# Optimization experiments

Measured on AMD Instinct MI355X. Metric: run time of the kernel, lower is better.

Reference implementation:

```python
import jax, jax.numpy as jnp
import numpy as np

EPS = 1e-5

def _branch(x, W, gamma, beta):
    # 1x1 conv (no bias) + InstanceNorm2d(affine) + ReLU
    y = jnp.einsum('oc,bchw->bohw', W, x)
    mu = y.mean(axis=(2, 3), keepdims=True)
    var = y.var(axis=(2, 3), keepdims=True)
    y = (y - mu) * jax.lax.rsqrt(var + EPS)
    y = y * gamma[None, :, None, None] + beta[None, :, None, None]
    return jax.nn.relu(y)

def setup_inputs() -> dict:
    key = jax.random.key(0)
    ks = jax.random.split(key, 12)
    b, in_ch, h, w = 2, 256, 64, 64
    c = in_ch // 8
    d = dict(
        x1=jax.random.normal(ks[0], (b, in_ch, h, w), jnp.float32),
        x2=jax.random.normal(ks[1], (b, in_ch, h, w), jnp.float32),
        x3=jax.random.normal(ks[2], (b, in_ch, h, w), jnp.float32),
        W1=jax.random.normal(ks[3], (c, in_ch), jnp.float32) * (1.0 / np.sqrt(in_ch)),
        g1=jnp.ones((c,), jnp.float32), b1=jnp.zeros((c,), jnp.float32),
        W2=jax.random.normal(ks[4], (c, in_ch), jnp.float32) * (1.0 / np.sqrt(in_ch)),
        g2=jnp.ones((c,), jnp.float32), b2=jnp.zeros((c,), jnp.float32),
        W3=jax.random.normal(ks[5], (c, in_ch), jnp.float32) * (1.0 / np.sqrt(in_ch)),
        g3=jnp.ones((c,), jnp.float32), b3=jnp.zeros((c,), jnp.float32),
    )
    return d

def _forward(x1, x2, x3, W1, g1, b1, W2, g2, b2, W3, g3, b3):
    q1 = _branch(x1, W1, g1, b1); q2 = _branch(x2, W1, g1, b1); q3 = _branch(x3, W1, g1, b1)
    k1 = _branch(x1, W2, g2, b2); k2 = _branch(x2, W2, g2, b2); k3 = _branch(x3, W2, g2, b2)
    v1 = _branch(x1, W3, g3, b3); v2 = _branch(x2, W3, g3, b3); v3 = _branch(x3, W3, g3, b3)
    b_, c, h, w = q1.shape
    hw = h * w
    Q1 = q1.reshape(b_, c, hw).transpose(0, 2, 1)  # [b,hw,c]
    Q2 = q2.reshape(b_, c, hw).transpose(0, 2, 1)
    Q3 = q3.reshape(b_, c, hw).transpose(0, 2, 1)
    K1 = k1.reshape(b_, c, hw)                      # [b,c,hw]
    K2 = k2.reshape(b_, c, hw)
    K3 = k3.reshape(b_, c, hw)
    sm = lambda Q, K: jax.nn.softmax(jnp.einsum('bic,bcj->bij', Q, K), axis=-1)
    A12 = sm(Q1, K2); A21 = sm(Q2, K1); A23 = sm(Q2, K3)
    A32 = sm(Q3, K2); A13 = sm(Q1, K3)
    # ones[b,c,hw] @ A == broadcast of column-sums of A: track a [b,hw] vector
    colsum = lambda A: A.sum(axis=1)                        # [b,hw]
    step = lambda v, A: jnp.einsum('bk,bkj->bj', v, A)      # [b,hw]
    def bc(v):  # broadcast [b,hw] -> [b,c,h,w]
        return jnp.broadcast_to(v[:, None, :], (b_, c, hw)).reshape(b_, c, h, w)
    p1a = bc(step(step(step(colsum(A12), A23), A32), A21))
    p1b = bc(step(colsum(A12), A21))
    p2 = bc(step(colsum(A23), A32))
    p3a = bc(step(colsum(A12), A23))
    p3b = bc(colsum(A13))
    return (p1a, p1b, p2, p3a, p3b, v1, v2, v3)

def reference(x1, x2, x3, W1, g1, b1, W2, g2, b2, W3, g3, b3):
    return _forward(x1, x2, x3, W1, g1, b1, W2, g2, b2, W3, g3, b3)
```

## Files before the change

### kernel.cpp

```cpp
#include <hip/hip_runtime.h>

typedef unsigned short u16;
typedef u16  u16x8  __attribute__((ext_vector_type(8)));
typedef _Float16 f16x4 __attribute__((ext_vector_type(4)));
typedef _Float16 f16x8 __attribute__((ext_vector_type(8)));
typedef float f32x4 __attribute__((ext_vector_type(4)));

#define HW 4096
#define CIN 256
#define HW32 (HW * 32)
#define L2E 1.4426950408889634f

__device__ __forceinline__ float fexp2(float x) { return __builtin_amdgcn_exp2f(x); }

__global__ __launch_bounds__(256) void convert_kernel(const float* x1, const float* x2, const float* x3,
        const float* W1, const float* W2, const float* W3,
        _Float16* xh, _Float16* wh, float* mean) {
    int bx = blockIdx.x; int t = threadIdx.x;
    if (bx < 1536) {
        int xi = bx >> 9, b = (bx >> 8) & 1, c = bx & 255;
        const float* src = (xi == 0 ? x1 : xi == 1 ? x2 : x3) + (size_t)(b * CIN + c) * HW;
        _Float16* dst = xh + ((size_t)((xi * 2 + b) * CIN) + c) * HW;
        float s = 0.f;
        for (int i = t; i < 1024; i += 256) {
            f32x4 v = ((const f32x4*)src)[i];
            s += v[0] + v[1] + v[2] + v[3];
            f16x4 h;
#pragma unroll
            for (int r = 0; r < 4; ++r) h[r] = (_Float16)v[r];
            ((f16x4*)dst)[i] = h;
        }
        __shared__ float red[256];
        red[t] = s; __syncthreads();
        for (int k = 128; k; k >>= 1) { if (t < k) red[t] += red[t + k]; __syncthreads(); }
        if (t == 0) mean[(xi * 2 + b) * CIN + c] = red[0] * (1.f / HW);
    } else {
        int j = bx - 1536;
        int widx = j >> 1, half = j & 1;
        const float* wsrc = (widx == 0 ? W1 : widx == 1 ? W2 : W3) + half * 4096;
        _Float16* wdst = wh + widx * 8192 + half * 4096;
        for (int i = t; i < 1024; i += 256) {
            f32x4 v = ((const f32x4*)wsrc)[i];
            f16x4 h;
#pragma unroll
            for (int r = 0; r < 4; ++r) h[r] = (_Float16)v[r];
            ((f16x4*)wdst)[i] = h;
        }
    }
}

__global__ __launch_bounds__(256) void m2_kernel(const _Float16* xh, float* M2) {
    int xi = blockIdx.y, b = blockIdx.z;
    const _Float16* xb = xh + (size_t)(xi * 2 + b) * CIN * HW;
    int t = threadIdx.x; int wv = t >> 6; int L = t & 63; int m = L & 15; int quad = L >> 4;
    int tile = blockIdx.x * 4 + wv;
    int c1t = (tile >> 4) * 16, c2t = (tile & 15) * 16;
    const f16x8* ap = (const f16x8*)(xb + (size_t)(c1t + m) * HW + quad * 8);
    const f16x8* bp = (const f16x8*)(xb + (size_t)(c2t + m) * HW + quad * 8);
    f32x4 a0 = {0,0,0,0}, a1 = {0,0,0,0};
#pragma unroll 4
    for (int p = 0; p < 128; p += 2) {
        a0 = __builtin_amdgcn_mfma_f32_16x16x32_f16(ap[p * 4], bp[p * 4], a0, 0, 0, 0);
        a1 = __builtin_amdgcn_mfma_f32_16x16x32_f16(ap[(p + 1) * 4], bp[(p + 1) * 4], a1, 0, 0, 0);
    }
    f32x4 acc = a0 + a1;
    float* dst = M2 + ((size_t)(xi * 2 + b) * CIN) * CIN;
#pragma unroll
    for (int r = 0; r < 4; ++r)
        dst[(size_t)(c1t + quad * 4 + r) * CIN + c2t + m] = acc[r] * (1.f / HW);
}

__global__ __launch_bounds__(256) void stats_kernel(const float* M2, const float* mean,
        const float* W1, const float* W2, const float* W3,
        const float* g1, const float* g2, const float* g3,
        const float* b1, const float* b2, const float* b3, float2* afine) {
    int o = blockIdx.x; int xi = blockIdx.y; int b = blockIdx.z;
    int widx = o >> 5; int oc = o & 31;
    const float* Wp = (widx == 0 ? W1 : widx == 1 ? W2 : W3) + oc * CIN;
    const float* gp = (widx == 0 ? g1 : widx == 1 ? g2 : g3);
    const float* bp = (widx == 0 ? b1 : widx == 1 ? b2 : b3);
    int t = threadIdx.x;
    __shared__ float sW[256];
    __shared__ float red[256];
    sW[t] = Wp[t];
    __syncthreads();
    const float* m2row = M2 + ((size_t)(xi * 2 + b) * CIN + t) * CIN;
    float tv = 0.f;
    const f32x4* r4 = (const f32x4*)m2row;
#pragma unroll 4
    for (int k = 0; k < 64; ++k) {
        f32x4 mv = r4[k];
        const f32x4 wv = *(const f32x4*)&sW[k * 4];
        tv += mv[0] * wv[0] + mv[1] * wv[1] + mv[2] * wv[2] + mv[3] * wv[3];
    }
    red[t] = tv * sW[t]; __syncthreads();
    for (int k = 128; k; k >>= 1) { if (t < k) red[t] += red[t + k]; __syncthreads(); }
    float E2 = red[0]; __syncthreads();
    red[t] = sW[t] * mean[(xi * 2 + b) * CIN + t]; __syncthreads();
    for (int k = 128; k; k >>= 1) { if (t < k) red[t] += red[t + k]; __syncthreads(); }
    if (t == 0) {
        float mu = red[0];
        float var = E2 - mu * mu;
        float rsig = rsqrtf(var + 1e-5f);
        float scale = gp[oc] * rsig;
        float bias = bp[oc] - mu * scale;
        if (widx == 0) { scale *= L2E; bias *= L2E; }
        afine[(xi * 2 + b) * 96 + o] = make_float2(scale, bias);
    }
}

__global__ __launch_bounds__(256) void conv_kernel(const _Float16* xh, const _Float16* wh,
        const float2* afine, _Float16* qT, _Float16* kT, float* out) {
    int xi = blockIdx.y, b = blockIdx.z;
    const u16* xb = (const u16*)(xh + (size_t)(xi * 2 + b) * CIN * HW);
    int p0 = blockIdx.x * 64;
    __shared__ u16 lds[32 * 65 * 8];
    int t = threadIdx.x;
    {
        int pc = t & 7, cg = t >> 3;
        u16x8 a[8];
#pragma unroll
        for (int r = 0; r < 8; ++r)
            a[r] = *(const u16x8*)(xb + (size_t)(cg * 8 + r) * HW + p0 + pc * 8);
#pragma unroll
        for (int i = 0; i < 8; ++i) {
            u16x8 d;
#pragma unroll
            for (int r = 0; r < 8; ++r) d[r] = a[r][i];
            int p = pc * 8 + i; int fp = p ^ (p >> 3);
            *(u16x8*)&lds[(cg * 65 + fp) * 8] = d;
        }
    }
    __syncthreads();
    int wv = t >> 6, L = t & 63, m = L & 15, quad = L >> 4;
    int pw0 = wv * 16;
    f16x8 af[8];
    {
        int p = pw0 + m; int fp = p ^ (p >> 3);
#pragma unroll
        for (int k = 0; k < 8; ++k)
            af[k] = *(const f16x8*)&lds[((k * 4 + quad) * 65 + fp) * 8];
    }
    int xb2 = xi * 2 + b;
    for (int ot = 0; ot < 6; ++ot) {
        int o0 = ot * 16; int widx = ot >> 1;
        int o_col = o0 + m;
        f32x4 acc = {0, 0, 0, 0};
#pragma unroll
        for (int k = 0; k < 8; ++k) {
            f16x8 bfr = *(const f16x8*)(wh + (size_t)o_col * CIN + k * 32 + quad * 8);
            acc = __builtin_amdgcn_mfma_f32_16x16x32_f16(af[k], bfr, acc, 0, 0, 0);
        }
        float2 afv = afine[xb2 * 96 + o_col];
        f32x4 vals;
#pragma unroll
        for (int r = 0; r < 4; ++r) {
            float v = acc[r] * afv.x + afv.y;
            vals[r] = v > 0.f ? v : 0.f;
        }
        int prow = p0 + pw0 + quad * 4;
        if (widx < 2) {
            _Float16* dst = (widx == 0 ? qT : kT) + (size_t)xb2 * HW32;
            int cc = (o0 & 31) + m;
#pragma unroll
            for (int r = 0; r < 4; ++r)
                dst[(size_t)(prow + r) * 32 + cc] = (_Float16)vals[r];
        } else {
            float* dst = out + (size_t)(5 + xi) * 262144 + (size_t)b * 131072 + (size_t)(o_col - 64) * HW + prow;
            *(f32x4*)dst = vals;
        }
    }
}

__global__ __launch_bounds__(256) void zsweep_kernel(const _Float16* qT, const _Float16* kT,
        float2* Pz) {
    const int qxA[5] = {0, 1, 1, 2, 0};
    const int kxA[5] = {1, 0, 2, 1, 2};
    int mat = blockIdx.y, b = blockIdx.z;
    const _Float16* qb = qT + (size_t)(qxA[mat] * 2 + b) * HW32;
    const _Float16* kb = kT + (size_t)(kxA[mat] * 2 + b) * HW32;
    int bx = blockIdx.x;
    int jc = bx & 15, qblk = bx >> 4;
    int t = threadIdx.x; int wv = t >> 6; int L = t & 63; int m = L & 15; int quad = L >> 4;
    int i0 = qblk * 256 + wv * 64;
    f16x8 a[4];
#pragma unroll
    for (int tt = 0; tt < 4; ++tt)
        a[tt] = *(const f16x8*)(qb + (size_t)(i0 + tt * 16 + m) * 32 + quad * 8);
    const f16x8* kp = (const f16x8*)(kb + m * 32 + quad * 8) + (size_t)jc * (16 * 64);
    f32x4 zero = {0.f, 0.f, 0.f, 0.f};
    f32x4 mx[4] = {zero, zero, zero, zero};
#pragma unroll 4
    for (int j = 0; j < 16; ++j) {
        f16x8 bf = kp[j * 64];
#pragma unroll
        for (int tt = 0; tt < 4; ++tt) {
            f32x4 d = __builtin_amdgcn_mfma_f32_16x16x32_f16(a[tt], bf, zero, 0, 0, 0);
            mx[tt][0] = fmaxf(mx[tt][0], d[0]); mx[tt][1] = fmaxf(mx[tt][1], d[1]);
            mx[tt][2] = fmaxf(mx[tt][2], d[2]); mx[tt][3] = fmaxf(mx[tt][3], d[3]);
        }
    }
#pragma unroll
    for (int tt = 0; tt < 4; ++tt)
#pragma unroll
        for (int msk = 1; msk <= 8; msk <<= 1) {
            mx[tt][0] = fmaxf(mx[tt][0], __shfl_xor(mx[tt][0], msk));
            mx[tt][1] = fmaxf(mx[tt][1], __shfl_xor(mx[tt][1], msk));
            mx[tt][2] = fmaxf(mx[tt][2], __shfl_xor(mx[tt][2], msk));
            mx[tt][3] = fmaxf(mx[tt][3], __shfl_xor(mx[tt][3], msk));
        }
    f32x4 neg[4];
#pragma unroll
    for (int tt = 0; tt < 4; ++tt) neg[tt] = -mx[tt];
    f32x4 z[4] = {zero, zero, zero, zero};
#pragma unroll 4
    for (int j = 0; j < 16; ++j) {
        f16x8 bf = kp[j * 64];
#pragma unroll
        for (int tt = 0; tt < 4; ++tt) {
            f32x4 d = __builtin_amdgcn_mfma_f32_16x16x32_f16(a[tt], bf, neg[tt], 0, 0, 0);
            z[tt][0] += fexp2(d[0]); z[tt][1] += fexp2(d[1]);
            z[tt][2] += fexp2(d[2]); z[tt][3] += fexp2(d[3]);
        }
    }
#pragma unroll
    for (int tt = 0; tt < 4; ++tt)
#pragma unroll
        for (int msk = 1; msk <= 8; msk <<= 1) {
            z[tt][0] += __shfl_xor(z[tt][0], msk); z[tt][1] += __shfl_xor(z[tt][1], msk);
            z[tt][2] += __shfl_xor(z[tt][2], msk); z[tt][3] += __shfl_xor(z[tt][3], msk);
        }
    if (m == 0) {
        int mb = mat * 2 + b;
#pragma unroll
        for (int tt = 0; tt < 4; ++tt) {
            int row = i0 + tt * 16 + quad * 4;
#pragma unroll
            for (int r = 0; r < 4; ++r)
                Pz[((size_t)mb * 16 + jc) * HW + row + r] = make_float2(mx[tt][r], z[tt][r]);
        }
    }
}

__global__ __launch_bounds__(256) void zcombine_kernel(const float2* Pz, float* R, float* Mv, float2* Wa) {
    int mb = blockIdx.y;
    int r = blockIdx.x * 256 + threadIdx.x;
    float2 p[16];
    float M = 0.f;
#pragma unroll
    for (int c = 0; c < 16; ++c) {
        p[c] = Pz[((size_t)mb * 16 + c) * HW + r];
        M = fmaxf(M, p[c].x);
    }
    float Z = 0.f;
#pragma unroll
    for (int c = 0; c < 16; ++c) Z += p[c].y * fexp2(p[c].x - M);
    float rz = 1.0f / Z;
    size_t idx = (size_t)mb * HW + r;
    R[idx] = rz; Mv[idx] = M;
    if (mb < 2 || mb >= 8) Wa[idx] = make_float2(rz, 0.f);
}

struct PCfg {
    const _Float16* qb; const _Float16* kb;
    const float* Mv;
    const float2* wt;
    float2* Pp;
    int nit;
};

__global__ __launch_bounds__(256) void pass2p_kernel(PCfg c0, PCfg c1) {
    PCfg c = (blockIdx.y == 0) ? c0 : c1;
    int b = blockIdx.z;
    int bx = blockIdx.x; int jb = bx & 15; int ic = bx >> 4;
    const _Float16* qb = c.qb + (size_t)b * HW32;
    const _Float16* kb = c.kb + (size_t)b * HW32;
    const float2* wt = c.wt + (size_t)b * HW;
    const float* Mb = c.Mv + (size_t)b * HW;
    int t = threadIdx.x; int wv = t >> 6; int L = t & 63; int m = L & 15; int quad = L >> 4;
    int j0 = jb * 256 + wv * 64;
    f16x8 bf[4];
#pragma unroll
    for (int tt = 0; tt < 4; ++tt)
        bf[tt] = *(const f16x8*)(kb + (size_t)(j0 + tt * 16 + m) * 32 + quad * 8);
    float a1[4] = {0, 0, 0, 0}, a2[4] = {0, 0, 0, 0};
    int ibase = ic * (c.nit * 16);
#pragma unroll 4
    for (int it = 0; it < c.nit; ++it) {
        int i0 = ibase + it * 16;
        f16x8 av = *(const f16x8*)(qb + (size_t)(i0 + m) * 32 + quad * 8);
        f32x4 Mr = *(const f32x4*)(Mb + i0 + quad * 4);
        f32x4 negM = -Mr;
        const float2* wr = wt + i0 + quad * 4;
        float2 w0 = wr[0], w1 = wr[1], w2 = wr[2], w3 = wr[3];
#pragma unroll
        for (int tt = 0; tt < 4; ++tt) {
            f32x4 d = __builtin_amdgcn_mfma_f32_16x16x32_f16(av, bf[tt], negM, 0, 0, 0);
            float e0 = fexp2(d[0]), e1 = fexp2(d[1]), e2 = fexp2(d[2]), e3 = fexp2(d[3]);
            a1[tt] += e0 * w0.x + e1 * w1.x + e2 * w2.x + e3 * w3.x;
            a2[tt] += e0 * w0.y + e1 * w1.y + e2 * w2.y + e3 * w3.y;
        }
    }
#pragma unroll
    for (int tt = 0; tt < 4; ++tt) {
        a1[tt] += __shfl_xor(a1[tt], 16); a1[tt] += __shfl_xor(a1[tt], 32);
        a2[tt] += __shfl_xor(a2[tt], 16); a2[tt] += __shfl_xor(a2[tt], 32);
    }
    if (quad == 0) {
        float2* dst = c.Pp + ((size_t)ic * 2 + b) * HW;
#pragma unroll
        for (int tt = 0; tt < 4; ++tt)
            dst[j0 + tt * 16 + m] = make_float2(a1[tt], a2[tt]);
    }
}

__global__ __launch_bounds__(256) void prepA_kernel(const float2* PpA, const float* R,
        float* c12, float* c13, float2* Wa2) {
    int b = blockIdx.y; int j = blockIdx.x * 256 + threadIdx.x;
    float s12 = 0.f, s13 = 0.f;
    for (int ic = 0; ic < 16; ++ic) {
        s12 += PpA[((size_t)ic * 2 + b) * HW + j].x;
        s13 += PpA[((size_t)(16 + ic) * 2 + b) * HW + j].x;
    }
    c12[(size_t)b * HW + j] = s12; c13[(size_t)b * HW + j] = s13;
    float rn = R[((size_t)(2 * 2 + b)) * HW + j];
    Wa2[(size_t)b * HW + j] = make_float2(rn, s12 * rn);
}

__global__ __launch_bounds__(256) void prep_kernel(const float2* Pp, const float* Rn,
        const float* aux, float* o1, float* o2, float2* Wn, int IC, int mode) {
    int b = blockIdx.y; int j = blockIdx.x * 256 + threadIdx.x;
    float s1 = 0.f, s2 = 0.f;
    for (int ic = 0; ic < IC; ++ic) {
        float2 p = Pp[((size_t)ic * 2 + b) * HW + j];
        s1 += p.x; s2 += p.y;
    }
    if (o1) o1[(size_t)b * HW + j] = s1;
    if (o2) o2[(size_t)b * HW + j] = s2;
    if (Wn) {
        float rn = Rn[(size_t)b * HW + j];
        float2 w = (mode == 0) ? make_float2(s1 * rn, s2 * rn)
                               : make_float2(s2 * rn, aux[(size_t)b * HW + j] * rn);
        Wn[(size_t)b * HW + j] = w;
    }
}

__global__ __launch_bounds__(256) void bcast_kernel(const float* vecs, float* out) {
    int bx = blockIdx.x;
    int s = bx >> 6; int rem = bx & 63; int b = rem >> 5; int c = rem & 31;
    const float* src = vecs + ((size_t)s * 2 + b) * HW;
    float* dst = out + ((size_t)(s * 2 + b) * 32 + c) * HW;
    int t = threadIdx.x;
#pragma unroll
    for (int k = 0; k < 4; ++k)
        ((f32x4*)dst)[k * 256 + t] = ((const f32x4*)src)[k * 256 + t];
}

extern "C" void kernel_launch(void* const* d_in, const int* in_sizes, int n_in,
                              void* d_out, int out_size, void* d_ws, size_t ws_size,
                              hipStream_t stream) {
    (void)in_sizes; (void)n_in; (void)out_size; (void)ws_size;
    const float* x1 = (const float*)d_in[0];
    const float* x2 = (const float*)d_in[1];
    const float* x3 = (const float*)d_in[2];
    const float* W1 = (const float*)d_in[3];
    const float* g1 = (const float*)d_in[4];
    const float* b1 = (const float*)d_in[5];
    const float* W2 = (const float*)d_in[6];
    const float* g2 = (const float*)d_in[7];
    const float* b2 = (const float*)d_in[8];
    const float* W3 = (const float*)d_in[9];
    const float* g3 = (const float*)d_in[10];
    const float* b3 = (const float*)d_in[11];
    float* out = (float*)d_out;

    char* w = (char*)d_ws;
    _Float16* xh    = (_Float16*)(w);
    _Float16* wh    = (_Float16*)(w + 12582912);
    float*    mean  = (float*)(w + 12632064);
    float*    M2    = (float*)(w + 12638208);
    float2*   afine = (float2*)(w + 14211072);
    _Float16* qT    = (_Float16*)(w + 14215680);
    _Float16* kT    = (_Float16*)(w + 15788544);
    float*    R     = (float*)(w + 17361408);
    float*    Mv    = (float*)(w + 17525248);
    float2*   Wa    = (float2*)(w + 17689088);
    float*    vecs  = (float*)(w + 18016768);
    float2*   Pz    = (float2*)(w + 18213376);
    float2*   PpA   = (float2*)(w + 23456256);
    float2*   PpB   = (float2*)(w + 25553408);
    float2*   PpC   = (float2*)(w + 27650560);
    float2*   PpD   = (float2*)(w + 29747712);

    float* v_p1a = vecs + 0 * 2 * HW;
    float* v_p1b = vecs + 1 * 2 * HW;
    float* v_p2  = vecs + 2 * 2 * HW;
    float* v_p3a = vecs + 3 * 2 * HW;
    float* v_p3b = vecs + 4 * 2 * HW;
    float* v_c12 = vecs + 5 * 2 * HW;

    hipLaunchKernelGGL(convert_kernel, dim3(1542), dim3(256), 0, stream,
                       x1, x2, x3, W1, W2, W3, xh, wh, mean);
    hipLaunchKernelGGL(m2_kernel, dim3(64, 3, 2), dim3(256), 0, stream, xh, M2);
    hipLaunchKernelGGL(stats_kernel, dim3(96, 3, 2), dim3(256), 0, stream,
                       M2, mean, W1, W2, W3, g1, g2, g3, b1, b2, b3, afine);
    hipLaunchKernelGGL(conv_kernel, dim3(64, 3, 2), dim3(256), 0, stream,
                       xh, wh, afine, qT, kT, out);
    hipLaunchKernelGGL(zsweep_kernel, dim3(256, 5, 2), dim3(256), 0, stream, qT, kT, Pz);
    hipLaunchKernelGGL(zcombine_kernel, dim3(16, 10), dim3(256), 0, stream, Pz, R, Mv, Wa);

    PCfg cA0 = { qT + 0 * 2 * HW32, kT + 1 * 2 * HW32, Mv + 0 * 2 * HW, Wa + 0 * 2 * HW, PpA,               16 };
    PCfg cA1 = { qT + 0 * 2 * HW32, kT + 2 * 2 * HW32, Mv + 4 * 2 * HW, Wa + 4 * 2 * HW, PpA + 16 * 2 * HW, 16 };
    hipLaunchKernelGGL(pass2p_kernel, dim3(256, 2, 2), dim3(256), 0, stream, cA0, cA1);
    hipLaunchKernelGGL(prepA_kernel, dim3(16, 2), dim3(256), 0, stream,
                       PpA, R, v_c12, v_p3b, Wa + 2 * 2 * HW);

    PCfg cB = { qT + 1 * 2 * HW32, kT + 2 * 2 * HW32, Mv + 2 * 2 * HW, Wa + 2 * 2 * HW, PpB, 8 };
    hipLaunchKernelGGL(pass2p_kernel, dim3(512, 1, 2), dim3(256), 0, stream, cB, cB);
    hipLaunchKernelGGL(prep_kernel, dim3(16, 2), dim3(256), 0, stream,
                       PpB, R + 3 * 2 * HW, (const float*)nullptr,
                       (float*)nullptr, v_p3a, Wa + 3 * 2 * HW, 32, 0);

    PCfg cC = { qT + 2 * 2 * HW32, kT + 1 * 2 * HW32, Mv + 3 * 2 * HW, Wa + 3 * 2 * HW, PpC, 8 };
    hipLaunchKernelGGL(pass2p_kernel, dim3(512, 1, 2), dim3(256), 0, stream, cC, cC);
    hipLaunchKernelGGL(prep_kernel, dim3(16, 2), dim3(256), 0, stream,
                       PpC, R + 1 * 2 * HW, v_c12,
                       v_p2, (float*)nullptr, Wa + 1 * 2 * HW, 32, 1);

    PCfg cD = { qT + 1 * 2 * HW32, kT + 0 * 2 * HW32, Mv + 1 * 2 * HW, Wa + 1 * 2 * HW, PpD, 8 };
    hipLaunchKernelGGL(pass2p_kernel, dim3(512, 1, 2), dim3(256), 0, stream, cD, cD);
    hipLaunchKernelGGL(prep_kernel, dim3(16, 2), dim3(256), 0, stream,
                       PpD, (const float*)nullptr, (const float*)nullptr,
                       v_p1a, v_p1b, (float2*)nullptr, 32, 0);

    hipLaunchKernelGGL(bcast_kernel, dim3(320), dim3(256), 0, stream, vecs, out);
}
```

Baseline: 320.7 us.

## Split Gram-matrix kernel over spatial chunks with 32x32 register tiles and combine pass

The channel Gram matrix (M2) kernel now splits the 4096-wide spatial reduction into 8 chunks and has each wave compute a 32x32 output region with four MFMA accumulators, so each loaded fragment is used twice. Partial sums go to a scratch buffer that reuses the Pz workspace, and a new combine kernel sums the 8 partials and scales by 1/HW. The aim is more parallelism across blocks and less global-load traffic per MFMA, at the cost of an extra kernel launch and a round trip of the partials through memory.

```diff
diff --git a/kernel.cpp b/kernel.cpp
--- a/kernel.cpp
+++ b/kernel.cpp
@@ -49,25 +49,48 @@
     }
 }
 
-__global__ __launch_bounds__(256) void m2_kernel(const _Float16* xh, float* M2) {
+__global__ __launch_bounds__(256) void m2_kernel(const _Float16* xh, float* Pm2) {
     int xi = blockIdx.y, b = blockIdx.z;
-    const _Float16* xb = xh + (size_t)(xi * 2 + b) * CIN * HW;
+    int xb = xi * 2 + b;
+    const _Float16* X = xh + (size_t)xb * CIN * HW;
+    int bx = blockIdx.x;
+    int chunk = bx >> 4, blk = bx & 15;
     int t = threadIdx.x; int wv = t >> 6; int L = t & 63; int m = L & 15; int quad = L >> 4;
-    int tile = blockIdx.x * 4 + wv;
-    int c1t = (tile >> 4) * 16, c2t = (tile & 15) * 16;
-    const f16x8* ap = (const f16x8*)(xb + (size_t)(c1t + m) * HW + quad * 8);
-    const f16x8* bp = (const f16x8*)(xb + (size_t)(c2t + m) * HW + quad * 8);
-    f32x4 a0 = {0,0,0,0}, a1 = {0,0,0,0};
+    int region = blk * 4 + wv;
+    int r1 = (region >> 3) * 32, r2 = (region & 7) * 32;
+    int p0 = chunk * 512 + quad * 8;
+    const f16x8* A0 = (const f16x8*)(X + (size_t)(r1 + m) * HW + p0);
+    const f16x8* A1 = (const f16x8*)(X + (size_t)(r1 + 16 + m) * HW + p0);
+    const f16x8* B0 = (const f16x8*)(X + (size_t)(r2 + m) * HW + p0);
+    const f16x8* B1 = (const f16x8*)(X + (size_t)(r2 + 16 + m) * HW + p0);
+    f32x4 zero = {0, 0, 0, 0};
+    f32x4 acc00 = zero, acc01 = zero, acc10 = zero, acc11 = zero;
 #pragma unroll 4
-    for (int p = 0; p < 128; p += 2) {
-        a0 = __builtin_amdgcn_mfma_f32_16x16x32_f16(ap[p * 4], bp[p * 4], a0, 0, 0, 0);
-        a1 = __builtin_amdgcn_mfma_f32_16x16x32_f16(ap[(p + 1) * 4], bp[(p + 1) * 4], a1, 0, 0, 0);
-    }
-    f32x4 acc = a0 + a1;
-    float* dst = M2 + ((size_t)(xi * 2 + b) * CIN) * CIN;
-#pragma unroll
-    for (int r = 0; r < 4; ++r)
-        dst[(size_t)(c1t + quad * 4 + r) * CIN + c2t + m] = acc[r] * (1.f / HW);
+    for (int it = 0; it < 16; ++it) {
+        f16x8 a0 = A0[it * 4], a1 = A1[it * 4];
+        f16x8 b0 = B0[it * 4], b1 = B1[it * 4];
+        acc00 = __builtin_amdgcn_mfma_f32_16x16x32_f16(a0, b0, acc00, 0, 0, 0);
+        acc01 = __builtin_amdgcn_mfma_f32_16x16x32_f16(a0, b1, acc01, 0, 0, 0);
+        acc10 = __builtin_amdgcn_mfma_f32_16x16x32_f16(a1, b0, acc10, 0, 0, 0);
+        acc11 = __builtin_amdgcn_mfma_f32_16x16x32_f16(a1, b1, acc11, 0, 0, 0);
+    }
+    float* dst = Pm2 + ((size_t)chunk * 6 + xb) * 65536;
+#pragma unroll
+    for (int r = 0; r < 4; ++r) {
+        int row0 = (r1 + quad * 4 + r) * 256, row1 = (r1 + 16 + quad * 4 + r) * 256;
+        dst[row0 + r2 + m] = acc00[r];
+        dst[row0 + r2 + 16 + m] = acc01[r];
+        dst[row1 + r2 + m] = acc10[r];
+        dst[row1 + r2 + 16 + m] = acc11[r];
+    }
+}
+
+__global__ __launch_bounds__(256) void m2combine_kernel(const float* Pm2, float* M2) {
+    size_t e = (size_t)blockIdx.x * 256 + threadIdx.x;
+    float s = 0.f;
+#pragma unroll
+    for (int c = 0; c < 8; ++c) s += Pm2[(size_t)c * 6 * 65536 + e];
+    M2[e] = s * (1.f / HW);
 }
 
 __global__ __launch_bounds__(256) void stats_kernel(const float* M2, const float* mean,
@@ -391,6 +414,7 @@
     float2*   PpB   = (float2*)(w + 25553408);
     float2*   PpC   = (float2*)(w + 27650560);
     float2*   PpD   = (float2*)(w + 29747712);
+    float*    Pm2   = (float*)(w + 18213376);
 
     float* v_p1a = vecs + 0 * 2 * HW;
     float* v_p1b = vecs + 1 * 2 * HW;
@@ -401,7 +425,8 @@
 
     hipLaunchKernelGGL(convert_kernel, dim3(1542), dim3(256), 0, stream,
                        x1, x2, x3, W1, W2, W3, xh, wh, mean);
-    hipLaunchKernelGGL(m2_kernel, dim3(64, 3, 2), dim3(256), 0, stream, xh, M2);
+    hipLaunchKernelGGL(m2_kernel, dim3(128, 3, 2), dim3(256), 0, stream, xh, Pm2);
+    hipLaunchKernelGGL(m2combine_kernel, dim3(1536), dim3(256), 0, stream, Pm2, M2);
     hipLaunchKernelGGL(stats_kernel, dim3(96, 3, 2), dim3(256), 0, stream,
                        M2, mean, W1, W2, W3, g1, g2, g3, b1, b2, b3, afine);
     hipLaunchKernelGGL(conv_kernel, dim3(64, 3, 2), dim3(256), 0, stream,
```

Result: faster. 293.3 us (-8.6%).
